# Optimization experiments

Measured on AMD Instinct MI355X. Metric: run time of the kernel, lower is better.

The kernel has to match this reference:

```python
import jax, jax.numpy as jnp
from jax import lax
import numpy as np

B, T, H = 128, 512, 512  # batch, seq_length, hidden_dim (== input_dim)


def _xavier(key, shape):
    fan_in, fan_out = shape[1], shape[0]
    limit = float(np.sqrt(6.0 / (fan_in + fan_out)))
    return jax.random.uniform(key, shape, jnp.float32, -limit, limit)


def setup_inputs() -> dict:
    key = jax.random.key(0)
    ks = jax.random.split(key, 10)
    s = 1.0 / np.sqrt(H)  # torch LSTM default init range
    return {
        "x": jax.random.normal(ks[0], (B, T, H), jnp.float32),
        "W_ih": jax.random.uniform(ks[1], (4 * H, H), jnp.float32, -s, s),
        "W_hh": jax.random.uniform(ks[2], (4 * H, H), jnp.float32, -s, s),
        "b_ih": jax.random.uniform(ks[3], (4 * H,), jnp.float32, -s, s),
        "b_hh": jax.random.uniform(ks[4], (4 * H,), jnp.float32, -s, s),
        "Ve": _xavier(ks[5], (1, H)),
        "U1": _xavier(ks[6], (H, 2 * H)),
        "U2": _xavier(ks[7], (H, H)),
        "W_out": _xavier(ks[8], (2, H)),
        "b_out": jnp.zeros((2,), jnp.float32),
    }


def _lstm(x, W_ih, W_hh, b_ih, b_hh):
    # x: [B, T, D] -> hidden states [B, T, H]; PyTorch gate order i,f,g,o
    b = b_ih + b_hh
    # precompute input projections for all timesteps: [T, B, 4H]
    xg = jnp.einsum('btd,gd->tbg', x, W_ih) + b

    def step(carry, xt):
        h, c = carry
        g = xt + h @ W_hh.T  # [B, 4H]
        i, f, gg, o = jnp.split(g, 4, axis=1)
        c = jax.nn.sigmoid(f) * c + jax.nn.sigmoid(i) * jnp.tanh(gg)
        h = jax.nn.sigmoid(o) * jnp.tanh(c)
        return (h, c), h

    h0 = jnp.zeros((x.shape[0], W_hh.shape[1]), x.dtype)
    (_, _), hs = lax.scan(step, (h0, h0), xg)
    return jnp.swapaxes(hs, 0, 1)  # [B, T, H]


def reference(x, W_ih, W_hh, b_ih, b_hh, Ve, U1, U2, W_out, b_out):
    h = _lstm(x, W_ih, W_hh, b_ih, b_hh)  # [B, T, H]
    h_last = h[:, -1, :]  # [B, H]
    # additive attention, vectorized over all timesteps
    Hdim = h.shape[-1]
    u1 = jnp.einsum('bth,gh->btg', h, U1[:, :Hdim]) + jnp.einsum('bh,gh->bg', h_last, U1[:, Hdim:])[:, None, :]
    u2 = jnp.einsum('btd,gd->btg', x, U2)
    u = jnp.tanh(u1 + u2)  # [B, T, H]
    e = jnp.einsum('bth,h->bt', u, Ve[0])
    alpha = jax.nn.softmax(e, axis=1)  # [B, T]
    context = jnp.einsum('bt,bth->bh', alpha, h)  # [B, H]
    params = context @ W_out.T + b_out  # [B, 2]
    mu = params[:, 0]
    sigma = jax.nn.softplus(params[:, 1]) + 1e-5
    return (mu, sigma)
```

## Files before the change

### kernel.cpp

```cpp
#include <hip/hip_runtime.h>
#include <stdint.h>


using short8  = __attribute__((ext_vector_type(8))) short;
using short4v = __attribute__((ext_vector_type(4))) short;
using floatx4 = __attribute__((ext_vector_type(4))) float;

#define MFMA16(a, b, c) __builtin_amdgcn_mfma_f32_16x16x32_bf16((a), (b), (c), 0, 0, 0)

__device__ __forceinline__ unsigned short f2b(float f) {
    unsigned u = __float_as_uint(f);
    u += 0x7FFFu + ((u >> 16) & 1u);
    return (unsigned short)(u >> 16);
}
__device__ __forceinline__ float b2f(unsigned short h) {
    return __uint_as_float(((unsigned)h) << 16);
}
__device__ __forceinline__ float sigm(float x) { return 1.0f / (1.0f + __expf(-x)); }
__device__ __forceinline__ float tanh_(float x) { return 1.0f - 2.0f / (__expf(2.0f * x) + 1.0f); }

__global__ __launch_bounds__(256) void prep(
    const float* __restrict__ x, const float* __restrict__ Wih, const float* __restrict__ Whh,
    const float* __restrict__ bih, const float* __restrict__ bhh,
    const float* __restrict__ U1, const float* __restrict__ U2,
    unsigned short* __restrict__ x_bf, unsigned short* __restrict__ Wih_bf,
    unsigned short* __restrict__ Whh_bf, unsigned short* __restrict__ U1a,
    unsigned short* __restrict__ U1b, unsigned short* __restrict__ U2b,
    float* __restrict__ bias)
{
    const long long NX4 = 33554432LL / 4;
    const long long NREST = 1048576LL + 1048576LL + 524288LL + 262144LL + 2048LL;
    const long long total = NX4 + NREST;
    for (long long u = (long long)blockIdx.x * 256 + threadIdx.x; u < total;
         u += (long long)gridDim.x * 256) {
        if (u < NX4) {
            float4 v = ((const float4*)x)[u];
            short4v o;
            o[0] = (short)f2b(v.x); o[1] = (short)f2b(v.y);
            o[2] = (short)f2b(v.z); o[3] = (short)f2b(v.w);
            *(short4v*)&x_bf[u * 4] = o;
        } else {
            long long i = u - NX4;
            if (i < 1048576) { Wih_bf[i] = f2b(Wih[i]); continue; }
            i -= 1048576;
            if (i < 1048576) { Whh_bf[i] = f2b(Whh[i]); continue; }
            i -= 1048576;
            if (i < 524288) {
                int row = (int)(i >> 10), col = (int)(i & 1023);
                if (col < 512) U1a[row * 512 + col] = f2b(U1[i]);
                else           U1b[row * 512 + (col - 512)] = f2b(U1[i]);
                continue;
            }
            i -= 524288;
            if (i < 262144) { U2b[i] = f2b(U2[i]); continue; }
            i -= 262144;
            bias[i] = bih[i] + bhh[i];
        }
    }
}

__device__ __forceinline__ void gemm_core(
    const unsigned short* __restrict__ A, long long lda,
    const unsigned short* __restrict__ Bm, long long ldb,
    unsigned short* __restrict__ C, long long ldc,
    const float* __restrict__ bias, int mode,
    int m0, int n0, int tid, unsigned short* sbuf)
{
    unsigned short* At = sbuf;
    unsigned short* Bt = sbuf + 128 * 72;
    unsigned short* Ct = sbuf;

    const int wv = tid >> 6, lane = tid & 63, l15 = lane & 15, q = lane >> 4;
    const int wm = wv & 1, wn = wv >> 1;

    floatx4 acc[4][4];
    for (int i = 0; i < 4; i++)
        for (int j = 0; j < 4; j++) acc[i][j] = (floatx4){0.f, 0.f, 0.f, 0.f};

    for (int k0 = 0; k0 < 512; k0 += 64) {
        for (int p = 0; p < 4; p++) {
            int idx = tid + p * 256;
            int row = idx >> 3, ch = idx & 7;
            *(short8*)&At[row * 72 + ch * 8] =
                *(const short8*)&A[(long long)(m0 + row) * lda + k0 + ch * 8];
            *(short8*)&Bt[row * 72 + ch * 8] =
                *(const short8*)&Bm[(long long)(n0 + row) * ldb + k0 + ch * 8];
        }
        __syncthreads();
        for (int ks = 0; ks < 64; ks += 32) {
            short8 af[4], bfv[4];
            for (int mi = 0; mi < 4; mi++)
                af[mi] = *(const short8*)&At[(wm * 64 + mi * 16 + l15) * 72 + ks + q * 8];
            for (int ni = 0; ni < 4; ni++)
                bfv[ni] = *(const short8*)&Bt[(wn * 64 + ni * 16 + l15) * 72 + ks + q * 8];
            for (int mi = 0; mi < 4; mi++)
                for (int ni = 0; ni < 4; ni++)
                    acc[mi][ni] = MFMA16(af[mi], bfv[ni], acc[mi][ni]);
        }
        __syncthreads();
    }

    float bv[4];
    for (int ni = 0; ni < 4; ni++)
        bv[ni] = bias ? bias[n0 + wn * 64 + ni * 16 + l15] : 0.0f;

    for (int mi = 0; mi < 4; mi++)
        for (int ni = 0; ni < 4; ni++)
            for (int r = 0; r < 4; r++)
                Ct[(wm * 64 + mi * 16 + q * 4 + r) * 128 + wn * 64 + ni * 16 + l15] =
                    f2b(acc[mi][ni][r] + bv[ni]);
    __syncthreads();

    const int tt0 = m0 & 511, bglob = m0 >> 9;
    for (int p = 0; p < 8; p++) {
        int idx = tid + p * 256;
        int row = idx >> 4, ch = idx & 15;
        if (mode) {
            int n = n0 + ch * 8;
            int gate = n >> 9, jg = (n >> 4) & 31, c0 = gate * 16 + (n & 15);
            long long dst = (((long long)(tt0 + row) * 32 + jg) * 128 + bglob) * 64 + c0;
            *(short8*)&C[dst] = *(const short8*)&Ct[row * 128 + ch * 8];
        } else {
            *(short8*)&C[(long long)(m0 + row) * ldc + n0 + ch * 8] =
                *(const short8*)&Ct[row * 128 + ch * 8];
        }
    }
}

__global__ __launch_bounds__(256) void gemm_bt(
    const unsigned short* __restrict__ A, long long lda,
    const unsigned short* __restrict__ Bm, long long ldb,
    unsigned short* __restrict__ C, long long ldc,
    const float* __restrict__ bias, int mode, int mmul)
{
    __shared__ __align__(16) unsigned short sbuf[2 * 128 * 72];
    gemm_core(A, lda, Bm, ldb, C, ldc, bias, mode,
              blockIdx.x * mmul, blockIdx.y * 128, threadIdx.x, sbuf);
}

#define GEMM_WGS 6144
__global__ __launch_bounds__(256, 1) void mega(
    const unsigned short* __restrict__ xg,
    const unsigned short* __restrict__ Whh,
    unsigned short* __restrict__ h_all,
    unsigned int* __restrict__ ring,
    const unsigned short* __restrict__ x_bf,
    const unsigned short* __restrict__ Wih_bf,
    const float* __restrict__ bias,
    unsigned short* __restrict__ xg_out,
    int* __restrict__ done)
{
    __shared__ __align__(16) char smem[36864];

    const int tid = threadIdx.x;

    if (blockIdx.x >= 64) {
        int g = blockIdx.x - 64;
        int b = g & 127;
        int r = g >> 7;
        int ti = 1 + (r % 3);
        int n = r / 3;
        gemm_core(x_bf, 512, Wih_bf, 512, xg_out, 2048, bias, 1,
                  b * 512 + ti * 128, n * 128, tid, (unsigned short*)smem);
        __syncthreads();
        if (tid == 0)
            __hip_atomic_fetch_add(done, 1, __ATOMIC_RELEASE,
                                   __HIP_MEMORY_SCOPE_AGENT);
        return;
    }

    unsigned int (*At)[16 * 264] = (unsigned int (*)[16 * 264])smem;

    const int wv = tid >> 6, lane = tid & 63, l15 = lane & 15, q = lane >> 4;
    const int bg = blockIdx.x >> 3, jgb = blockIdx.x & 7;
    const int b0 = bg * 16;
    const int jg32 = jgb * 4 + wv;
    const int hid = jg32 * 16 + l15;

    short8 Wreg[4][16];
    #pragma unroll
    for (int ct = 0; ct < 4; ct++)
        #pragma unroll
        for (int kk = 0; kk < 16; kk++)
            Wreg[ct][kk] = *(const short8*)
                &Whh[(long long)(ct * 512 + hid) * 512 + kk * 32 + q * 8];

    float cst[4] = {0.f, 0.f, 0.f, 0.f};

    for (int t = 0; t < 512; t++) {
        if (t == 128) {
            if (tid == 0) {
                while (__hip_atomic_load(done, __ATOMIC_ACQUIRE,
                                         __HIP_MEMORY_SCOPE_AGENT) < GEMM_WGS)
                    __builtin_amdgcn_s_sleep(8);
            }
            __syncthreads();
        }
        const long long xbase = ((long long)(t * 32 + jg32) * 128 + b0) * 64;
        floatx4 acc[4];
        #pragma unroll
        for (int ct = 0; ct < 4; ct++)
            #pragma unroll
            for (int r = 0; r < 4; r++)
                acc[ct][r] = b2f(xg[xbase + (q * 4 + r) * 64 + ct * 16 + l15]);

        if (t > 0) {
            const unsigned want = (unsigned)(t - 1);
            const int sl = (t - 1) & 1;
            unsigned long long* rb = (unsigned long long*)
                (ring + sl * 65536 + b0 * 512);
            unsigned long long w[16];
            #pragma unroll
            for (int i = 0; i < 16; i++)
                w[i] = __hip_atomic_load(&rb[tid + i * 256], __ATOMIC_RELAXED,
                                         __HIP_MEMORY_SCOPE_AGENT);
            while (true) {
                unsigned bad = 0;
                #pragma unroll
                for (int i = 0; i < 16; i++) {
                    unsigned lo = (unsigned)(w[i] >> 16) & 0xFFFFu;
                    unsigned hi = (unsigned)(w[i] >> 48);
                    bad |= (lo ^ want) | (hi ^ want);
                }
                if (!bad) break;
                #pragma unroll
                for (int i = 0; i < 16; i++) {
                    unsigned lo = (unsigned)(w[i] >> 16) & 0xFFFFu;
                    unsigned hi = (unsigned)(w[i] >> 48);
                    if ((lo ^ want) | (hi ^ want))
                        w[i] = __hip_atomic_load(&rb[tid + i * 256], __ATOMIC_RELAXED,
                                                 __HIP_MEMORY_SCOPE_AGENT);
                }
            }
            unsigned int* dst = &At[sl][0];
            #pragma unroll
            for (int i = 0; i < 16; i++) {
                int idx = tid + i * 256;
                int row = idx >> 8, k = idx & 255;
                dst[row * 264 + k] =
                    (unsigned)(w[i] & 0xFFFFu) | ((unsigned)(w[i] >> 32) << 16);
            }
            __syncthreads();
            const unsigned int* ap = &At[sl][l15 * 264 + q * 4];
            #pragma unroll
            for (int kk = 0; kk < 16; kk++) {
                short8 af = *(const short8*)(ap + kk * 16);
                acc[0] = MFMA16(af, Wreg[0][kk], acc[0]);
                acc[1] = MFMA16(af, Wreg[1][kk], acc[1]);
                acc[2] = MFMA16(af, Wreg[2][kk], acc[2]);
                acc[3] = MFMA16(af, Wreg[3][kk], acc[3]);
            }
        }
        unsigned short hbv[4];
        #pragma unroll
        for (int r = 0; r < 4; r++) {
            float ig = sigm(acc[0][r]);
            float fg = sigm(acc[1][r]);
            float gv = tanh_(acc[2][r]);
            float og = sigm(acc[3][r]);
            cst[r] = fg * cst[r] + ig * gv;
            hbv[r] = f2b(og * tanh_(cst[r]));
        }
        #pragma unroll
        for (int r = 0; r < 4; r++) {
            const int b = b0 + q * 4 + r;
            __hip_atomic_store(&ring[(t & 1) * 65536 + b * 512 + hid],
                               ((unsigned)t << 16) | hbv[r], __ATOMIC_RELAXED,
                               __HIP_MEMORY_SCOPE_AGENT);
        }
        #pragma unroll
        for (int r = 0; r < 4; r++) {
            const int b = b0 + q * 4 + r;
            h_all[(long long)b * 262144 + (long long)t * 512 + hid] = hbv[r];
        }
    }
}

__global__ __launch_bounds__(256) void attn_e(
    const unsigned short* __restrict__ h_all,
    const unsigned short* __restrict__ x_bf,
    const unsigned short* __restrict__ U1a, const unsigned short* __restrict__ U2b,
    const unsigned short* __restrict__ u1b,
    const float* __restrict__ Ve,
    float* __restrict__ e)
{
    __shared__ __align__(16) unsigned short Bt[512 * 40];
    __shared__ __align__(16) unsigned short At[32 * 40];
    __shared__ float ered[4][32];

    const int tid = threadIdx.x;
    const int wv = tid >> 6, lane = tid & 63, l15 = lane & 15, q = lane >> 4;
    const int b = blockIdx.x >> 4, t0 = (blockIdx.x & 15) * 32;

    floatx4 acc[2][8];
    for (int mi = 0; mi < 2; mi++)
        for (int ni = 0; ni < 8; ni++) acc[mi][ni] = (floatx4){0.f, 0.f, 0.f, 0.f};

    for (int it = 0; it < 32; it++) {
        const int phase = it >> 4, kk = (it & 15) * 32;
        const unsigned short* Asrc = phase ? x_bf : h_all;
        const unsigned short* Bsrc = phase ? U2b : U1a;
        __syncthreads();
        for (int idx = tid; idx < 2048; idx += 256) {
            int row = idx >> 2, ch = idx & 3;
            *(short8*)&Bt[row * 40 + ch * 8] =
                *(const short8*)&Bsrc[(long long)row * 512 + kk + ch * 8];
        }
        if (tid < 128) {
            int row = tid >> 2, ch = tid & 3;
            *(short8*)&At[row * 40 + ch * 8] =
                *(const short8*)&Asrc[(long long)(b * 512 + t0 + row) * 512 + kk + ch * 8];
        }
        __syncthreads();
        short8 af[2];
        for (int mi = 0; mi < 2; mi++)
            af[mi] = *(const short8*)&At[(mi * 16 + l15) * 40 + q * 8];
        for (int ni = 0; ni < 8; ni++) {
            short8 bfv = *(const short8*)&Bt[(wv * 128 + ni * 16 + l15) * 40 + q * 8];
            acc[0][ni] = MFMA16(af[0], bfv, acc[0][ni]);
            acc[1][ni] = MFMA16(af[1], bfv, acc[1][ni]);
        }
    }

    float s[2][4] = {{0.f, 0.f, 0.f, 0.f}, {0.f, 0.f, 0.f, 0.f}};
    for (int ni = 0; ni < 8; ni++) {
        int n = wv * 128 + ni * 16 + l15;
        float ub = b2f(u1b[b * 512 + n]);
        float vev = Ve[n];
        for (int mi = 0; mi < 2; mi++)
            for (int r = 0; r < 4; r++)
                s[mi][r] += vev * tanh_(acc[mi][ni][r] + ub);
    }
    for (int off = 1; off <= 8; off <<= 1)
        for (int mi = 0; mi < 2; mi++)
            for (int r = 0; r < 4; r++) s[mi][r] += __shfl_xor(s[mi][r], off);
    if (l15 == 0)
        for (int mi = 0; mi < 2; mi++)
            for (int r = 0; r < 4; r++) ered[wv][mi * 16 + q * 4 + r] = s[mi][r];
    __syncthreads();
    if (tid < 32)
        e[(long long)b * 512 + t0 + tid] =
            ered[0][tid] + ered[1][tid] + ered[2][tid] + ered[3][tid];
}

__global__ __launch_bounds__(256) void attn_out(
    const float* __restrict__ e, const unsigned short* __restrict__ h_all,
    const float* __restrict__ Wout, const float* __restrict__ bout,
    float* __restrict__ outp)
{
    __shared__ float sm[512];
    __shared__ float red[8];
    const int b = blockIdx.x, tid = threadIdx.x;
    const int wv = tid >> 6, lane = tid & 63;

    float e0 = e[b * 512 + tid], e1 = e[b * 512 + 256 + tid];
    float mx = fmaxf(e0, e1);
    for (int off = 32; off; off >>= 1) mx = fmaxf(mx, __shfl_xor(mx, off));
    if (lane == 0) red[wv] = mx;
    __syncthreads();
    mx = fmaxf(fmaxf(red[0], red[1]), fmaxf(red[2], red[3]));

    float s0 = __expf(e0 - mx), s1 = __expf(e1 - mx);
    sm[tid] = s0; sm[256 + tid] = s1;
    float ss = s0 + s1;
    for (int off = 32; off; off >>= 1) ss += __shfl_xor(ss, off);
    if (lane == 0) red[4 + wv] = ss;
    __syncthreads();
    float inv = 1.0f / (red[4] + red[5] + red[6] + red[7]);

    const unsigned int* hp = (const unsigned int*)(h_all + (long long)b * 262144);
    float a0 = 0.f, a1 = 0.f;
    for (int t = 0; t < 512; t += 4) {
        #pragma unroll
        for (int j = 0; j < 4; j++) {
            float al = sm[t + j];
            unsigned v = hp[(t + j) * 256 + tid];
            a0 += al * b2f((unsigned short)(v & 0xFFFFu));
            a1 += al * b2f((unsigned short)(v >> 16));
        }
    }
    a0 *= inv; a1 *= inv;

    float q0 = a0 * Wout[2 * tid] + a1 * Wout[2 * tid + 1];
    float q1 = a0 * Wout[512 + 2 * tid] + a1 * Wout[512 + 2 * tid + 1];
    for (int off = 32; off; off >>= 1) { q0 += __shfl_xor(q0, off); q1 += __shfl_xor(q1, off); }
    __syncthreads();
    if (lane == 0) { red[wv] = q0; red[4 + wv] = q1; }
    __syncthreads();
    if (tid == 0) {
        float P0 = red[0] + red[1] + red[2] + red[3] + bout[0];
        float P1 = red[4] + red[5] + red[6] + red[7] + bout[1];
        outp[b] = P0;
        float sp = (P1 > 15.0f) ? P1 : log1pf(__expf(P1));
        outp[128 + b] = sp + 1e-5f;
    }
}

extern "C" void kernel_launch(void* const* d_in, const int* in_sizes, int n_in,
                              void* d_out, int out_size, void* d_ws, size_t ws_size,
                              hipStream_t stream)
{
    const float* x    = (const float*)d_in[0];
    const float* Wih  = (const float*)d_in[1];
    const float* Whh  = (const float*)d_in[2];
    const float* bih  = (const float*)d_in[3];
    const float* bhh  = (const float*)d_in[4];
    const float* Ve   = (const float*)d_in[5];
    const float* U1   = (const float*)d_in[6];
    const float* U2   = (const float*)d_in[7];
    const float* Wout = (const float*)d_in[8];
    const float* bout = (const float*)d_in[9];
    float* out = (float*)d_out;

    char* ws = (char*)d_ws;
    size_t off = 0;
    auto alloc = [&](size_t bytes) -> void* {
        void* p = ws + off;
        off += (bytes + 255) & ~(size_t)255;
        return p;
    };
    unsigned short* x_bf   = (unsigned short*)alloc(33554432ull * 2);
    unsigned short* Wih_bf = (unsigned short*)alloc(1048576ull * 2);
    unsigned short* Whh_bf = (unsigned short*)alloc(1048576ull * 2);
    unsigned short* U1a    = (unsigned short*)alloc(262144ull * 2);
    unsigned short* U1b    = (unsigned short*)alloc(262144ull * 2);
    unsigned short* U2b    = (unsigned short*)alloc(262144ull * 2);
    float*          bias   = (float*)alloc(2048ull * 4);
    unsigned short* xg     = (unsigned short*)alloc(134217728ull * 2);
    unsigned short* h_all  = (unsigned short*)alloc(33554432ull * 2);
    unsigned short* u1bv   = (unsigned short*)alloc(65536ull * 2);
    float*          e      = (float*)alloc(65536ull * 4);
    unsigned int*   ring   = (unsigned int*)alloc(131072ull * 4);
    int*            done   = (int*)alloc(256ull);
    if (off > ws_size) return;

    hipMemsetAsync(done, 0, 4, stream);
    prep<<<4096, 256, 0, stream>>>(x, Wih, Whh, bih, bhh, U1, U2,
                                   x_bf, Wih_bf, Whh_bf, U1a, U1b, U2b, bias);
    gemm_bt<<<dim3(128, 16), 256, 0, stream>>>(x_bf, 512, Wih_bf, 512,
                                               xg, 2048, bias, 1, 512);
    mega<<<64 + GEMM_WGS, 256, 0, stream>>>(xg, Whh_bf, h_all, ring,
                                            x_bf, Wih_bf, bias, xg, done);
    gemm_bt<<<dim3(1, 4), 256, 0, stream>>>(h_all + 511 * 512, 262144, U1b, 512,
                                            u1bv, 512, nullptr, 0, 128);
    attn_e<<<2048, 256, 0, stream>>>(h_all, x_bf, U1a, U2b, u1bv, Ve, e);
    attn_out<<<128, 256, 0, stream>>>(e, h_all, Wout, bout, out);
}
```

Before: 2.746 ms.

## Overlap attention GEMM with LSTM recurrence inside persistent mega kernel

Moves the attention projection GEMM (h·U1a + x·U2) into extra workgroups of the persistent mega kernel. These wait on per-batch-group progress counters and write fp32 pre-activations into the dead xg buffer, so the work overlaps the serial recurrence. The per-segment xg GEMM completion is now tracked with three counters so the recurrence waits only for the chunk it needs. The recurrence also prefetches ring data earlier, splits the MFMA chain into two accumulators, raises its priority and writes h in paired 32-bit stores. The tanh/Ve reduction moves into attn_out, which removes the attn_e launch, at the cost of more contention with the latency-critical recurrence and more complex cross-block synchronisation.

```diff
diff --git a/kernel.cpp b/kernel.cpp
--- a/kernel.cpp
+++ b/kernel.cpp
@@ -139,6 +139,7 @@
 }
 
 #define GEMM_WGS 6144
+#define ATTN_WGS 2048
 __global__ __launch_bounds__(256, 1) void mega(
     const unsigned short* __restrict__ xg,
     const unsigned short* __restrict__ Whh,
@@ -148,26 +149,100 @@
     const unsigned short* __restrict__ Wih_bf,
     const float* __restrict__ bias,
     unsigned short* __restrict__ xg_out,
-    int* __restrict__ done)
+    int* __restrict__ syncp,
+    const unsigned short* __restrict__ U1a,
+    const unsigned short* __restrict__ U2b)
 {
     __shared__ __align__(16) char smem[36864];
 
     const int tid = threadIdx.x;
 
-    if (blockIdx.x >= 64) {
+    if (blockIdx.x >= 64 && blockIdx.x < 64 + GEMM_WGS) {
         int g = blockIdx.x - 64;
-        int b = g & 127;
-        int r = g >> 7;
-        int ti = 1 + (r % 3);
-        int n = r / 3;
+        int ti = 1 + (g >> 11);
+        int r2 = g & 2047;
+        int b = r2 & 127;
+        int n = r2 >> 7;
         gemm_core(x_bf, 512, Wih_bf, 512, xg_out, 2048, bias, 1,
                   b * 512 + ti * 128, n * 128, tid, (unsigned short*)smem);
         __syncthreads();
         if (tid == 0)
-            __hip_atomic_fetch_add(done, 1, __ATOMIC_RELEASE,
+            __hip_atomic_fetch_add(&syncp[ti - 1], 1, __ATOMIC_RELEASE,
                                    __HIP_MEMORY_SCOPE_AGENT);
         return;
     }
+
+    if (blockIdx.x >= 64 + GEMM_WGS) {
+        const int g = blockIdx.x - 64 - GEMM_WGS;
+        const int tt = g >> 7;
+        const int b  = g & 127;
+        const int t0 = tt * 32;
+        const int bg = b >> 4;
+
+        if (tid < 8) {
+            while (__hip_atomic_load(&syncp[8 + bg * 8 + tid], __ATOMIC_RELAXED,
+                                     __HIP_MEMORY_SCOPE_AGENT) < t0 + 32)
+                __builtin_amdgcn_s_sleep(8);
+        }
+        __syncthreads();
+
+        unsigned short* Bt2 = (unsigned short*)smem;
+        unsigned short* At2 = (unsigned short*)smem + 512 * 32;
+
+        const int wv = tid >> 6, lane = tid & 63, l15 = lane & 15, q = lane >> 4;
+
+        floatx4 acc[2][8];
+        for (int mi = 0; mi < 2; mi++)
+            for (int ni = 0; ni < 8; ni++) acc[mi][ni] = (floatx4){0.f, 0.f, 0.f, 0.f};
+
+        for (int it = 0; it < 32; it++) {
+            const int phase = it >> 4, kk = (it & 15) * 32;
+            const unsigned short* Bsrc = phase ? U2b : U1a;
+            __syncthreads();
+            for (int idx = tid; idx < 2048; idx += 256) {
+                int row = idx >> 2, ch = idx & 3;
+                *(short8*)&Bt2[row * 32 + ch * 8] =
+                    *(const short8*)&Bsrc[(long long)row * 512 + kk + ch * 8];
+            }
+            if (tid < 128) {
+                int row = tid >> 2, ch = tid & 3;
+                if (phase == 0) {
+                    unsigned long long* p = (unsigned long long*)
+                        &h_all[((long long)b * 512 + t0 + row) * 512 + kk + ch * 8];
+                    unsigned long long lo = __hip_atomic_load(p, __ATOMIC_RELAXED,
+                                                              __HIP_MEMORY_SCOPE_AGENT);
+                    unsigned long long hi = __hip_atomic_load(p + 1, __ATOMIC_RELAXED,
+                                                              __HIP_MEMORY_SCOPE_AGENT);
+                    unsigned long long* d = (unsigned long long*)&At2[row * 40 + ch * 8];
+                    d[0] = lo; d[1] = hi;
+                } else {
+                    *(short8*)&At2[row * 40 + ch * 8] =
+                        *(const short8*)&x_bf[((long long)b * 512 + t0 + row) * 512 + kk + ch * 8];
+                }
+            }
+            __syncthreads();
+            short8 af0 = *(const short8*)&At2[(l15) * 40 + q * 8];
+            short8 af1 = *(const short8*)&At2[(16 + l15) * 40 + q * 8];
+            for (int ni = 0; ni < 8; ni++) {
+                short8 bfv = *(const short8*)&Bt2[(wv * 128 + ni * 16 + l15) * 32 + q * 8];
+                acc[0][ni] = MFMA16(af0, bfv, acc[0][ni]);
+                acc[1][ni] = MFMA16(af1, bfv, acc[1][ni]);
+            }
+        }
+        for (int mi = 0; mi < 2; mi++)
+            for (int ni = 0; ni < 8; ni++) {
+                const int n = wv * 128 + ni * 16 + l15;
+                #pragma unroll
+                for (int r = 0; r < 4; r++) {
+                    const int t = t0 + mi * 16 + q * 4 + r;
+                    float* slot = (float*)&xg_out[(((long long)t * 32 + (n >> 5)) * 128 + b) * 64];
+                    slot[n & 31] = acc[mi][ni][r];
+                }
+            }
+        return;
+    }
+
+    __builtin_amdgcn_s_setprio(1);
 
     unsigned int (*At)[16 * 264] = (unsigned int (*)[16 * 264])smem;
 
@@ -188,14 +263,27 @@
     float cst[4] = {0.f, 0.f, 0.f, 0.f};
 
     for (int t = 0; t < 512; t++) {
-        if (t == 128) {
+        if (t == 128 || t == 256 || t == 384) {
             if (tid == 0) {
-                while (__hip_atomic_load(done, __ATOMIC_ACQUIRE,
-                                         __HIP_MEMORY_SCOPE_AGENT) < GEMM_WGS)
+                const int gi = (t >> 7) - 1;
+                while (__hip_atomic_load(&syncp[gi], __ATOMIC_ACQUIRE,
+                                         __HIP_MEMORY_SCOPE_AGENT) < 2048)
                     __builtin_amdgcn_s_sleep(8);
             }
             __syncthreads();
         }
+
+        unsigned long long w[16];
+        const int sl = (t - 1) & 1;
+        unsigned long long* rb = (unsigned long long*)
+            (ring + sl * 65536 + b0 * 512);
+        if (t > 0) {
+            #pragma unroll
+            for (int i = 0; i < 16; i++)
+                w[i] = __hip_atomic_load(&rb[tid + i * 256], __ATOMIC_RELAXED,
+                                         __HIP_MEMORY_SCOPE_AGENT);
+        }
+
         const long long xbase = ((long long)(t * 32 + jg32) * 128 + b0) * 64;
         floatx4 acc[4];
         #pragma unroll
@@ -203,17 +291,12 @@
             #pragma unroll
             for (int r = 0; r < 4; r++)
                 acc[ct][r] = b2f(xg[xbase + (q * 4 + r) * 64 + ct * 16 + l15]);
+        floatx4 acc2[4];
+        #pragma unroll
+        for (int ct = 0; ct < 4; ct++) acc2[ct] = (floatx4){0.f, 0.f, 0.f, 0.f};
 
         if (t > 0) {
             const unsigned want = (unsigned)(t - 1);
-            const int sl = (t - 1) & 1;
-            unsigned long long* rb = (unsigned long long*)
-                (ring + sl * 65536 + b0 * 512);
-            unsigned long long w[16];
-            #pragma unroll
-            for (int i = 0; i < 16; i++)
-                w[i] = __hip_atomic_load(&rb[tid + i * 256], __ATOMIC_RELAXED,
-                                         __HIP_MEMORY_SCOPE_AGENT);
             while (true) {
                 unsigned bad = 0;
                 #pragma unroll
@@ -243,21 +326,26 @@
             __syncthreads();
             const unsigned int* ap = &At[sl][l15 * 264 + q * 4];
             #pragma unroll
-            for (int kk = 0; kk < 16; kk++) {
-                short8 af = *(const short8*)(ap + kk * 16);
+            for (int kk = 0; kk < 8; kk++) {
+                short8 af  = *(const short8*)(ap + kk * 16);
+                short8 af2 = *(const short8*)(ap + (kk + 8) * 16);
                 acc[0] = MFMA16(af, Wreg[0][kk], acc[0]);
                 acc[1] = MFMA16(af, Wreg[1][kk], acc[1]);
                 acc[2] = MFMA16(af, Wreg[2][kk], acc[2]);
                 acc[3] = MFMA16(af, Wreg[3][kk], acc[3]);
+                acc2[0] = MFMA16(af2, Wreg[0][kk + 8], acc2[0]);
+                acc2[1] = MFMA16(af2, Wreg[1][kk + 8], acc2[1]);
+                acc2[2] = MFMA16(af2, Wreg[2][kk + 8], acc2[2]);
+                acc2[3] = MFMA16(af2, Wreg[3][kk + 8], acc2[3]);
             }
         }
         unsigned short hbv[4];
         #pragma unroll
         for (int r = 0; r < 4; r++) {
-            float ig = sigm(acc[0][r]);
-            float fg = sigm(acc[1][r]);
-            float gv = tanh_(acc[2][r]);
-            float og = sigm(acc[3][r]);
+            float ig = sigm(acc[0][r] + acc2[0][r]);
+            float fg = sigm(acc[1][r] + acc2[1][r]);
+            float gv = tanh_(acc[2][r] + acc2[2][r]);
+            float og = sigm(acc[3][r] + acc2[3][r]);
             cst[r] = fg * cst[r] + ig * gv;
             hbv[r] = f2b(og * tanh_(cst[r]));
         }
@@ -271,89 +359,72 @@
         #pragma unroll
         for (int r = 0; r < 4; r++) {
             const int b = b0 + q * 4 + r;
-            h_all[(long long)b * 262144 + (long long)t * 512 + hid] = hbv[r];
-        }
-    }
-}
-
-__global__ __launch_bounds__(256) void attn_e(
+            int o = __shfl_xor((int)hbv[r], 1);
+            if (!(l15 & 1)) {
+                unsigned v = (unsigned)hbv[r] | (((unsigned)(unsigned short)o) << 16);
+                __hip_atomic_store(
+                    (unsigned*)&h_all[(long long)b * 262144 + (long long)t * 512 + hid],
+                    v, __ATOMIC_RELAXED, __HIP_MEMORY_SCOPE_AGENT);
+            }
+        }
+        if ((t & 15) == 15) {
+            __syncthreads();
+            if (tid == 0)
+                __hip_atomic_store(&syncp[8 + (int)blockIdx.x], t + 1,
+                                   __ATOMIC_RELAXED, __HIP_MEMORY_SCOPE_AGENT);
+        }
+    }
+}
+
+__global__ __launch_bounds__(256) void attn_out(
+    const unsigned short* __restrict__ a_xg,
     const unsigned short* __restrict__ h_all,
-    const unsigned short* __restrict__ x_bf,
-    const unsigned short* __restrict__ U1a, const unsigned short* __restrict__ U2b,
-    const unsigned short* __restrict__ u1b,
+    const unsigned short* __restrict__ u1bv,
     const float* __restrict__ Ve,
-    float* __restrict__ e)
-{
-    __shared__ __align__(16) unsigned short Bt[512 * 40];
-    __shared__ __align__(16) unsigned short At[32 * 40];
-    __shared__ float ered[4][32];
-
-    const int tid = threadIdx.x;
-    const int wv = tid >> 6, lane = tid & 63, l15 = lane & 15, q = lane >> 4;
-    const int b = blockIdx.x >> 4, t0 = (blockIdx.x & 15) * 32;
-
-    floatx4 acc[2][8];
-    for (int mi = 0; mi < 2; mi++)
-        for (int ni = 0; ni < 8; ni++) acc[mi][ni] = (floatx4){0.f, 0.f, 0.f, 0.f};
-
-    for (int it = 0; it < 32; it++) {
-        const int phase = it >> 4, kk = (it & 15) * 32;
-        const unsigned short* Asrc = phase ? x_bf : h_all;
-        const unsigned short* Bsrc = phase ? U2b : U1a;
-        __syncthreads();
-        for (int idx = tid; idx < 2048; idx += 256) {
-            int row = idx >> 2, ch = idx & 3;
-            *(short8*)&Bt[row * 40 + ch * 8] =
-                *(const short8*)&Bsrc[(long long)row * 512 + kk + ch * 8];
-        }
-        if (tid < 128) {
-            int row = tid >> 2, ch = tid & 3;
-            *(short8*)&At[row * 40 + ch * 8] =
-                *(const short8*)&Asrc[(long long)(b * 512 + t0 + row) * 512 + kk + ch * 8];
-        }
-        __syncthreads();
-        short8 af[2];
-        for (int mi = 0; mi < 2; mi++)
-            af[mi] = *(const short8*)&At[(mi * 16 + l15) * 40 + q * 8];
-        for (int ni = 0; ni < 8; ni++) {
-            short8 bfv = *(const short8*)&Bt[(wv * 128 + ni * 16 + l15) * 40 + q * 8];
-            acc[0][ni] = MFMA16(af[0], bfv, acc[0][ni]);
-            acc[1][ni] = MFMA16(af[1], bfv, acc[1][ni]);
-        }
-    }
-
-    float s[2][4] = {{0.f, 0.f, 0.f, 0.f}, {0.f, 0.f, 0.f, 0.f}};
-    for (int ni = 0; ni < 8; ni++) {
-        int n = wv * 128 + ni * 16 + l15;
-        float ub = b2f(u1b[b * 512 + n]);
-        float vev = Ve[n];
-        for (int mi = 0; mi < 2; mi++)
-            for (int r = 0; r < 4; r++)
-                s[mi][r] += vev * tanh_(acc[mi][ni][r] + ub);
-    }
-    for (int off = 1; off <= 8; off <<= 1)
-        for (int mi = 0; mi < 2; mi++)
-            for (int r = 0; r < 4; r++) s[mi][r] += __shfl_xor(s[mi][r], off);
-    if (l15 == 0)
-        for (int mi = 0; mi < 2; mi++)
-            for (int r = 0; r < 4; r++) ered[wv][mi * 16 + q * 4 + r] = s[mi][r];
-    __syncthreads();
-    if (tid < 32)
-        e[(long long)b * 512 + t0 + tid] =
-            ered[0][tid] + ered[1][tid] + ered[2][tid] + ered[3][tid];
-}
-
-__global__ __launch_bounds__(256) void attn_out(
-    const float* __restrict__ e, const unsigned short* __restrict__ h_all,
     const float* __restrict__ Wout, const float* __restrict__ bout,
     float* __restrict__ outp)
 {
+    __shared__ float se[512];
     __shared__ float sm[512];
     __shared__ float red[8];
     const int b = blockIdx.x, tid = threadIdx.x;
     const int wv = tid >> 6, lane = tid & 63;
 
-    float e0 = e[b * 512 + tid], e1 = e[b * 512 + 256 + tid];
+    const int n0 = lane * 8;
+    float ve[8], ub[8];
+    #pragma unroll
+    for (int j = 0; j < 8; j++) {
+        ve[j] = Ve[n0 + j];
+        ub[j] = b2f(u1bv[b * 512 + n0 + j]);
+    }
+    for (int it = 0; it < 64; it++) {
+        const int t = it * 8 + wv * 2;
+        const float* s0p = (const float*)
+            &a_xg[(((long long)t * 32 + (n0 >> 5)) * 128 + b) * 64];
+        const float* s1p = (const float*)
+            &a_xg[(((long long)(t + 1) * 32 + (n0 >> 5)) * 128 + b) * 64];
+        float4 a0 = *(const float4*)&s0p[n0 & 31];
+        float4 a1 = *(const float4*)&s0p[(n0 & 31) + 4];
+        float4 a2 = *(const float4*)&s1p[n0 & 31];
+        float4 a3 = *(const float4*)&s1p[(n0 & 31) + 4];
+        float s0 = ve[0] * tanh_(a0.x + ub[0]) + ve[1] * tanh_(a0.y + ub[1])
+                 + ve[2] * tanh_(a0.z + ub[2]) + ve[3] * tanh_(a0.w + ub[3])
+                 + ve[4] * tanh_(a1.x + ub[4]) + ve[5] * tanh_(a1.y + ub[5])
+                 + ve[6] * tanh_(a1.z + ub[6]) + ve[7] * tanh_(a1.w + ub[7]);
+        float s1 = ve[0] * tanh_(a2.x + ub[0]) + ve[1] * tanh_(a2.y + ub[1])
+                 + ve[2] * tanh_(a2.z + ub[2]) + ve[3] * tanh_(a2.w + ub[3])
+                 + ve[4] * tanh_(a3.x + ub[4]) + ve[5] * tanh_(a3.y + ub[5])
+                 + ve[6] * tanh_(a3.z + ub[6]) + ve[7] * tanh_(a3.w + ub[7]);
+        #pragma unroll
+        for (int off = 1; off <= 32; off <<= 1) {
+            s0 += __shfl_xor(s0, off);
+            s1 += __shfl_xor(s1, off);
+        }
+        if (lane == 0) { se[t] = s0; se[t + 1] = s1; }
+    }
+    __syncthreads();
+
+    float e0 = se[tid], e1 = se[256 + tid];
     float mx = fmaxf(e0, e1);
     for (int off = 32; off; off >>= 1) mx = fmaxf(mx, __shfl_xor(mx, off));
     if (lane == 0) red[wv] = mx;
@@ -429,20 +500,18 @@
     unsigned short* xg     = (unsigned short*)alloc(134217728ull * 2);
     unsigned short* h_all  = (unsigned short*)alloc(33554432ull * 2);
     unsigned short* u1bv   = (unsigned short*)alloc(65536ull * 2);
-    float*          e      = (float*)alloc(65536ull * 4);
     unsigned int*   ring   = (unsigned int*)alloc(131072ull * 4);
-    int*            done   = (int*)alloc(256ull);
+    int*            syncp  = (int*)alloc(512ull);
     if (off > ws_size) return;
 
-    hipMemsetAsync(done, 0, 4, stream);
+    hipMemsetAsync(syncp, 0, 512, stream);
     prep<<<4096, 256, 0, stream>>>(x, Wih, Whh, bih, bhh, U1, U2,
                                    x_bf, Wih_bf, Whh_bf, U1a, U1b, U2b, bias);
     gemm_bt<<<dim3(128, 16), 256, 0, stream>>>(x_bf, 512, Wih_bf, 512,
                                                xg, 2048, bias, 1, 512);
-    mega<<<64 + GEMM_WGS, 256, 0, stream>>>(xg, Whh_bf, h_all, ring,
-                                            x_bf, Wih_bf, bias, xg, done);
+    mega<<<64 + GEMM_WGS + ATTN_WGS, 256, 0, stream>>>(
+        xg, Whh_bf, h_all, ring, x_bf, Wih_bf, bias, xg, syncp, U1a, U2b);
     gemm_bt<<<dim3(1, 4), 256, 0, stream>>>(h_all + 511 * 512, 262144, U1b, 512,
                                             u1bv, 512, nullptr, 0, 128);
-    attn_e<<<2048, 256, 0, stream>>>(h_all, x_bf, U1a, U2b, u1bv, Ve, e);
-    attn_out<<<128, 256, 0, stream>>>(e, h_all, Wout, bout, out);
-}
+    attn_out<<<128, 256, 0, stream>>>(xg, h_all, u1bv, Ve, Wout, bout, out);
+}
```

Result: slower. 2.913 ms (+6.1%).

## Fuse U1 attention projection of hidden states into recurrent LSTM kernel

Applied to the files above, without the earlier changes.

Each recurrent workgroup keeps a slice of U1a in shared memory. It reuses the per-step hidden-state fragments already staged for the W_hh MFMAs to compute h·U1a^T. The fp32 results go into the already-consumed xg slots of the previous timestep. The attention-score kernel then only computes the x·U2 half and reads the precomputed U1 term, roughly halving its GEMM work. The cost is an extra MFMA per k-step and extra stores on the serial recurrence path, plus about 66 KB more LDS for the mega kernel, which also limits occupancy of the co-scheduled input-projection GEMM workgroups.

```diff
diff --git a/kernel.cpp b/kernel.cpp
--- a/kernel.cpp
+++ b/kernel.cpp
@@ -148,9 +148,11 @@
     const unsigned short* __restrict__ Wih_bf,
     const float* __restrict__ bias,
     unsigned short* __restrict__ xg_out,
-    int* __restrict__ done)
+    int* __restrict__ done,
+    const unsigned short* __restrict__ U1a)
 {
     __shared__ __align__(16) char smem[36864];
+    __shared__ __align__(16) unsigned short U1s[64 * 520];
 
     const int tid = threadIdx.x;
 
@@ -177,6 +179,14 @@
     const int jg32 = jgb * 4 + wv;
     const int hid = jg32 * 16 + l15;
 
+    #pragma unroll
+    for (int p = 0; p < 16; p++) {
+        int idx = tid + p * 256;
+        int row = idx >> 6, ch = idx & 63;
+        *(short8*)&U1s[row * 520 + ch * 8] =
+            *(const short8*)&U1a[(long long)(jgb * 64 + row) * 512 + ch * 8];
+    }
+
     short8 Wreg[4][16];
     #pragma unroll
     for (int ct = 0; ct < 4; ct++)
@@ -186,6 +196,10 @@
                 &Whh[(long long)(ct * 512 + hid) * 512 + kk * 32 + q * 8];
 
     float cst[4] = {0.f, 0.f, 0.f, 0.f};
+
+    const int jgp = jgb * 2 + (wv >> 1);
+    const int c0a = (wv & 1) * 16 + l15;
+    const unsigned short* u1p = &U1s[(wv * 16 + l15) * 520 + q * 8];
 
     for (int t = 0; t < 512; t++) {
         if (t == 128) {
@@ -203,6 +217,8 @@
             #pragma unroll
             for (int r = 0; r < 4; r++)
                 acc[ct][r] = b2f(xg[xbase + (q * 4 + r) * 64 + ct * 16 + l15]);
+
+        floatx4 acc_a = (floatx4){0.f, 0.f, 0.f, 0.f};
 
         if (t > 0) {
             const unsigned want = (unsigned)(t - 1);
@@ -249,6 +265,8 @@
                 acc[1] = MFMA16(af, Wreg[1][kk], acc[1]);
                 acc[2] = MFMA16(af, Wreg[2][kk], acc[2]);
                 acc[3] = MFMA16(af, Wreg[3][kk], acc[3]);
+                short8 uf = *(const short8*)(u1p + kk * 32);
+                acc_a = MFMA16(af, uf, acc_a);
             }
         }
         unsigned short hbv[4];
@@ -273,14 +291,75 @@
             const int b = b0 + q * 4 + r;
             h_all[(long long)b * 262144 + (long long)t * 512 + hid] = hbv[r];
         }
-    }
-}
-
-__global__ __launch_bounds__(256) void attn_e(
-    const unsigned short* __restrict__ h_all,
+        if (t > 0) {
+            #pragma unroll
+            for (int r = 0; r < 4; r++) {
+                const int b = b0 + q * 4 + r;
+                float* slot = (float*)&xg_out[(((long long)(t - 1) * 32 + jgp) * 128 + b) * 64];
+                slot[c0a] = acc_a[r];
+            }
+        }
+    }
+
+    {
+        const unsigned want = 511u;
+        const int sl = 1;
+        unsigned long long* rb = (unsigned long long*)
+            (ring + sl * 65536 + b0 * 512);
+        unsigned long long w[16];
+        #pragma unroll
+        for (int i = 0; i < 16; i++)
+            w[i] = __hip_atomic_load(&rb[tid + i * 256], __ATOMIC_RELAXED,
+                                     __HIP_MEMORY_SCOPE_AGENT);
+        while (true) {
+            unsigned bad = 0;
+            #pragma unroll
+            for (int i = 0; i < 16; i++) {
+                unsigned lo = (unsigned)(w[i] >> 16) & 0xFFFFu;
+                unsigned hi = (unsigned)(w[i] >> 48);
+                bad |= (lo ^ want) | (hi ^ want);
+            }
+            if (!bad) break;
+            #pragma unroll
+            for (int i = 0; i < 16; i++) {
+                unsigned lo = (unsigned)(w[i] >> 16) & 0xFFFFu;
+                unsigned hi = (unsigned)(w[i] >> 48);
+                if ((lo ^ want) | (hi ^ want))
+                    w[i] = __hip_atomic_load(&rb[tid + i * 256], __ATOMIC_RELAXED,
+                                             __HIP_MEMORY_SCOPE_AGENT);
+            }
+        }
+        unsigned int* dst = &At[sl][0];
+        #pragma unroll
+        for (int i = 0; i < 16; i++) {
+            int idx = tid + i * 256;
+            int row = idx >> 8, k = idx & 255;
+            dst[row * 264 + k] =
+                (unsigned)(w[i] & 0xFFFFu) | ((unsigned)(w[i] >> 32) << 16);
+        }
+        __syncthreads();
+        const unsigned int* ap = &At[sl][l15 * 264 + q * 4];
+        floatx4 acc_a = (floatx4){0.f, 0.f, 0.f, 0.f};
+        #pragma unroll
+        for (int kk = 0; kk < 16; kk++) {
+            short8 af = *(const short8*)(ap + kk * 16);
+            short8 uf = *(const short8*)(u1p + kk * 32);
+            acc_a = MFMA16(af, uf, acc_a);
+        }
+        #pragma unroll
+        for (int r = 0; r < 4; r++) {
+            const int b = b0 + q * 4 + r;
+            float* slot = (float*)&xg_out[(((long long)511 * 32 + jgp) * 128 + b) * 64];
+            slot[c0a] = acc_a[r];
+        }
+    }
+}
+
+__global__ __launch_bounds__(256) void attn_e2(
+    const unsigned short* __restrict__ a_xg,
     const unsigned short* __restrict__ x_bf,
-    const unsigned short* __restrict__ U1a, const unsigned short* __restrict__ U2b,
-    const unsigned short* __restrict__ u1b,
+    const unsigned short* __restrict__ U2b,
+    const unsigned short* __restrict__ u1bv,
     const float* __restrict__ Ve,
     float* __restrict__ e)
 {
@@ -296,20 +375,18 @@
     for (int mi = 0; mi < 2; mi++)
         for (int ni = 0; ni < 8; ni++) acc[mi][ni] = (floatx4){0.f, 0.f, 0.f, 0.f};
 
-    for (int it = 0; it < 32; it++) {
-        const int phase = it >> 4, kk = (it & 15) * 32;
-        const unsigned short* Asrc = phase ? x_bf : h_all;
-        const unsigned short* Bsrc = phase ? U2b : U1a;
+    for (int it = 0; it < 16; it++) {
+        const int kk = it * 32;
         __syncthreads();
         for (int idx = tid; idx < 2048; idx += 256) {
             int row = idx >> 2, ch = idx & 3;
             *(short8*)&Bt[row * 40 + ch * 8] =
-                *(const short8*)&Bsrc[(long long)row * 512 + kk + ch * 8];
+                *(const short8*)&U2b[(long long)row * 512 + kk + ch * 8];
         }
         if (tid < 128) {
             int row = tid >> 2, ch = tid & 3;
             *(short8*)&At[row * 40 + ch * 8] =
-                *(const short8*)&Asrc[(long long)(b * 512 + t0 + row) * 512 + kk + ch * 8];
+                *(const short8*)&x_bf[(long long)(b * 512 + t0 + row) * 512 + kk + ch * 8];
         }
         __syncthreads();
         short8 af[2];
@@ -324,12 +401,18 @@
 
     float s[2][4] = {{0.f, 0.f, 0.f, 0.f}, {0.f, 0.f, 0.f, 0.f}};
     for (int ni = 0; ni < 8; ni++) {
-        int n = wv * 128 + ni * 16 + l15;
-        float ub = b2f(u1b[b * 512 + n]);
-        float vev = Ve[n];
-        for (int mi = 0; mi < 2; mi++)
-            for (int r = 0; r < 4; r++)
-                s[mi][r] += vev * tanh_(acc[mi][ni][r] + ub);
+        const int n = wv * 128 + ni * 16 + l15;
+        const float ub = b2f(u1bv[b * 512 + n]);
+        const float vev = Ve[n];
+        const int jgp = n >> 5, c0 = n & 31;
+        for (int mi = 0; mi < 2; mi++) {
+            #pragma unroll
+            for (int r = 0; r < 4; r++) {
+                const int t = t0 + mi * 16 + q * 4 + r;
+                float av = ((const float*)&a_xg[(((long long)t * 32 + jgp) * 128 + b) * 64])[c0];
+                s[mi][r] += vev * tanh_(acc[mi][ni][r] + av + ub);
+            }
+        }
     }
     for (int off = 1; off <= 8; off <<= 1)
         for (int mi = 0; mi < 2; mi++)
@@ -440,9 +523,9 @@
     gemm_bt<<<dim3(128, 16), 256, 0, stream>>>(x_bf, 512, Wih_bf, 512,
                                                xg, 2048, bias, 1, 512);
     mega<<<64 + GEMM_WGS, 256, 0, stream>>>(xg, Whh_bf, h_all, ring,
-                                            x_bf, Wih_bf, bias, xg, done);
+                                            x_bf, Wih_bf, bias, xg, done, U1a);
     gemm_bt<<<dim3(1, 4), 256, 0, stream>>>(h_all + 511 * 512, 262144, U1b, 512,
                                             u1bv, 512, nullptr, 0, 128);
-    attn_e<<<2048, 256, 0, stream>>>(h_all, x_bf, U1a, U2b, u1bv, Ve, e);
+    attn_e2<<<2048, 256, 0, stream>>>(xg, x_bf, U2b, u1bv, Ve, e);
     attn_out<<<128, 256, 0, stream>>>(e, h_all, Wout, bout, out);
 }
```

Measured after the change: 2.709 ms. Within noise of the previous version (-1.3%).
